# Kernel optimization log

Measured on AMD Instinct MI355X. Metric: run time of the kernel, lower is better.

The kernel has to match this reference:

```python
import jax, jax.numpy as jnp
import numpy as np

IMG, P, C = 512, 16, 1
D, DEPTH, H, DH, MLP = 768, 12, 8, 64, 2048
GRID = IMG // P          # 32
NP = GRID * GRID         # 1024 patches
N = NP + 1               # +cls token
EPS = 1e-5


def _ln(x, s, b):
    m = jnp.mean(x, -1, keepdims=True)
    v = jnp.mean((x - m) ** 2, -1, keepdims=True)
    return (x - m) * jax.lax.rsqrt(v + EPS) * s + b


def setup_inputs() -> dict:
    key = jax.random.key(0)
    ks = jax.random.split(key, 12)
    s = 0.02
    f32 = jnp.float32
    return {
        "x": jax.random.normal(ks[0], (4, C, IMG, IMG), f32),
        "conv_w": jax.random.normal(ks[1], (D, C, P, P), f32) * s,   # [out,in,kh,kw] like torch
        "conv_b": jnp.zeros((D,), f32),
        "cls_token": jax.random.normal(ks[2], (1, 1, D), f32),
        "pos_emb": jax.random.normal(ks[3], (1, N, D), f32),
        "qkv_w": jax.random.normal(ks[4], (DEPTH, D, 3 * H * DH), f32) * s,  # [in,out] layout
        "merge_w": jax.random.normal(ks[5], (DEPTH, H * DH, D), f32) * s,
        "merge_b": jnp.zeros((DEPTH, D), f32),
        "ln1_s": jnp.ones((DEPTH, D), f32),
        "ln1_b": jnp.zeros((DEPTH, D), f32),
        "ln2_s": jnp.ones((DEPTH, D), f32),
        "ln2_b": jnp.zeros((DEPTH, D), f32),
        "ffn_w1": jax.random.normal(ks[6], (DEPTH, D, MLP), f32) * s,
        "ffn_b1": jnp.zeros((DEPTH, MLP), f32),
        "ffn_w2": jax.random.normal(ks[7], (DEPTH, MLP, D), f32) * s,
        "ffn_b2": jnp.zeros((DEPTH, D), f32),
        "lnf_s": jnp.ones((D,), f32),
        "lnf_b": jnp.zeros((D,), f32),
    }


def reference(x, conv_w, conv_b, cls_token, pos_emb, qkv_w, merge_w, merge_b,
              ln1_s, ln1_b, ln2_s, ln2_b, ffn_w1, ffn_b1, ffn_w2, ffn_b2,
              lnf_s, lnf_b):
    B = x.shape[0]
    # Patch embed: stride-P conv == non-overlapping patch extraction + matmul
    xr = x.reshape(B, C, GRID, P, GRID, P)
    tok = jnp.einsum('bchpwq,dcpq->bhwd', xr, conv_w).reshape(B, NP, D) + conv_b
    t = jnp.concatenate([jnp.broadcast_to(cls_token, (B, 1, D)), tok], axis=1)
    t = t + pos_emb  # dropout is identity in eval
    scale = DH ** -0.5
    for i in range(DEPTH):
        # MSA with pre-LN
        h = _ln(t, ln1_s[i], ln1_b[i])
        qkv = (h @ qkv_w[i]).reshape(B, N, H, 3, DH)   # [B,N,H,3,DH]
        q = jnp.transpose(qkv[..., 0, :], (0, 2, 1, 3))  # [B,H,N,DH]
        k = jnp.transpose(qkv[..., 1, :], (0, 2, 1, 3))
        v = jnp.transpose(qkv[..., 2, :], (0, 2, 1, 3))
        att = jax.nn.softmax(jnp.einsum('bhnd,bhmd->bhnm', q, k) * scale, axis=-1)
        o = jnp.einsum('bhnm,bhmd->bhnd', att, v)
        o = jnp.transpose(o, (0, 2, 1, 3)).reshape(B, N, H * DH)
        t = t + (o @ merge_w[i] + merge_b[i])
        # FFN with pre-LN, exact (erf) GELU like torch nn.GELU
        h2 = _ln(t, ln2_s[i], ln2_b[i])
        f = jax.nn.gelu(h2 @ ffn_w1[i] + ffn_b1[i], approximate=False)
        t = t + (f @ ffn_w2[i] + ffn_b2[i])
    return _ln(t, lnf_s, lnf_b)
```

## Files before the change

### kernel.cpp

```cpp
#include <hip/hip_runtime.h>

#define DEV __device__ __forceinline__

typedef short s8v __attribute__((ext_vector_type(8)));
typedef float f4v __attribute__((ext_vector_type(4)));

DEV short f2bf(float f) {
  unsigned u = __float_as_uint(f);
  u += 0x7FFFu + ((u >> 16) & 1u);
  return (short)(u >> 16);
}
DEV short f2bf_fast(float f) {
  return (short)((__float_as_uint(f) + 0x8000u) >> 16);
}
DEV float bf2f(short s) { return __uint_as_float(((unsigned)(unsigned short)s) << 16); }

DEV void gld_lds16(const short* g, short* l) {
  __builtin_amdgcn_global_load_lds(
      (const __attribute__((address_space(1))) void*)g,
      (__attribute__((address_space(3))) void*)l, 16, 0, 0);
}

DEV int xcd_swz(int id, int nwg) {
  int q8 = nwg >> 3, r8 = nwg & 7, xcd = id & 7, off = id >> 3;
  return (xcd < r8) ? (xcd * (q8 + 1) + off) : (r8 * (q8 + 1) + (xcd - r8) * q8 + off);
}

template<int BN>
__global__ __launch_bounds__(256) void gemm_t(
    const short* __restrict__ A, const short* __restrict__ B, void* __restrict__ Cv,
    const float* __restrict__ bias,
    int M, int N, int K, int lda, int ldb, int ldc, int flags)
{
  constexpr int BPASS = BN / 32;
  constexpr int MI = (BN == 128) ? 4 : 2;
  __shared__ __align__(16) short As[2][64 * 64];
  __shared__ __align__(16) short Bs[2][BN * 64];
  int nwg = gridDim.x * gridDim.y;
  int idl = blockIdx.y * gridDim.x + blockIdx.x;
  int swz = xcd_swz(idl, nwg);
  int bx = swz % gridDim.x, by = swz / gridDim.x;
  int m0 = by * 64, n0 = bx * BN;
  int tid = threadIdx.x, lane = tid & 63, w = tid >> 6;
  int lr = lane & 15, kg = lane >> 4;
  int wrb = (BN == 128) ? 0 : (w >> 1) * 32;
  int wcb = (BN == 128) ? w * 32 : (w & 1) * 32;
  f4v acc[MI][2] = {};
  int NT = K >> 6;

#define STAGE(bufi, k0)                                                   \
  {                                                                       \
    _Pragma("unroll")                                                     \
    for (int p = 0; p < 2; ++p) {                                         \
      int ch = p * 256 + w * 64 + lane;                                   \
      int row = ch >> 3, c = (ch & 7) ^ (row & 7);                        \
      gld_lds16(A + (long)(m0 + row) * lda + (k0) + c * 8,                \
                &As[bufi][(p * 256 + w * 64) * 8]);                       \
    }                                                                     \
    _Pragma("unroll")                                                     \
    for (int p = 0; p < BPASS; ++p) {                                     \
      int ch = p * 256 + w * 64 + lane;                                   \
      int row = ch >> 3, c = (ch & 7) ^ (row & 7);                        \
      gld_lds16(B + (long)(n0 + row) * ldb + (k0) + c * 8,                \
                &Bs[bufi][(p * 256 + w * 64) * 8]);                       \
    }                                                                     \
  }

  STAGE(0, 0)
  for (int t = 0; t < NT; ++t) {
    int buf = t & 1;
    if (t + 1 < NT) {
      STAGE(buf ^ 1, (t + 1) * 64)
      if constexpr (BN == 128)
        asm volatile("s_waitcnt vmcnt(6)" ::: "memory");
      else
        asm volatile("s_waitcnt vmcnt(4)" ::: "memory");
    } else {
      asm volatile("s_waitcnt vmcnt(0)" ::: "memory");
    }
    __builtin_amdgcn_s_barrier();
    #pragma unroll
    for (int ks = 0; ks < 2; ++ks) {
      s8v av[MI], bv[2];
      #pragma unroll
      for (int mi = 0; mi < MI; ++mi) {
        int row = wrb + mi * 16 + lr;
        int sl = (ks * 4 + kg) ^ (row & 7);
        av[mi] = *(const s8v*)&As[buf][row * 64 + sl * 8];
      }
      #pragma unroll
      for (int ni = 0; ni < 2; ++ni) {
        int row = wcb + ni * 16 + lr;
        int sl = (ks * 4 + kg) ^ (row & 7);
        bv[ni] = *(const s8v*)&Bs[buf][row * 64 + sl * 8];
      }
      #pragma unroll
      for (int mi = 0; mi < MI; ++mi)
        #pragma unroll
        for (int ni = 0; ni < 2; ++ni)
          acc[mi][ni] = __builtin_amdgcn_mfma_f32_16x16x32_bf16(av[mi], bv[ni], acc[mi][ni], 0, 0, 0);
    }
    asm volatile("s_waitcnt lgkmcnt(0)" ::: "memory");
    __builtin_amdgcn_s_barrier();
  }
#undef STAGE

  float* Cf = (float*)Cv;
  short* Cb = (short*)Cv;
  #pragma unroll
  for (int mi = 0; mi < MI; ++mi)
    #pragma unroll
    for (int ni = 0; ni < 2; ++ni) {
      int col = n0 + wcb + ni * 16 + lr;
      float bvv = (flags & 1) ? bias[col] : 0.f;
      #pragma unroll
      for (int j = 0; j < 4; ++j) {
        int row = m0 + wrb + mi * 16 + kg * 4 + j;
        if (row >= M) continue;
        float v = acc[mi][ni][j] + bvv;
        if (flags & 2) v = 0.5f * v * (1.f + erff(v * 0.70710678118f));
        long ci = (long)row * ldc + col;
        if (flags & 8) Cb[ci] = f2bf(v);
        else { if (flags & 4) v += Cf[ci]; Cf[ci] = v; }
      }
    }
}

__global__ __launch_bounds__(256) void flash_k(
    const short* __restrict__ qkv, short* __restrict__ O)
{
  int swz = xcd_swz(blockIdx.x, 544);
  int z = swz / 17, qt = swz - z * 17;
  int zb = z >> 3, zh = z & 7;
  const short* base = qkv + (long)zb * 1025 * 1536 + zh * 192;
  const short* Qg = base;
  const short* Kg = base + 64;
  const short* Vg = base + 128;
  int q0 = qt * 64;
  int tid = threadIdx.x, lane = tid & 63, w = tid >> 6;
  int lr = lane & 15, kg = lane >> 4;

  __shared__ __align__(16) short QPs[64][72];
  __shared__ __align__(16) short Ks[2][64 * 64];
  __shared__ __align__(16) short Vt[2][64][72];

  for (int s = tid; s < 512; s += 256) {
    int row = s >> 3, ch = s & 7;
    s8v v = {};
    if (q0 + row < 1025) v = *(const s8v*)(Qg + (long)(q0 + row) * 1536 + ch * 8);
    *(s8v*)&QPs[row][ch * 8] = v;
  }
  __syncthreads();
  s8v aq[2];
  aq[0] = *(const s8v*)&QPs[w * 16 + lr][kg * 8];
  aq[1] = *(const s8v*)&QPs[w * 16 + lr][32 + kg * 8];

#define STAGE_K(bufi, kv0)                                                 \
  {                                                                        \
    int s0 = w * 128;                                                      \
    _Pragma("unroll")                                                      \
    for (int i = 0; i < 2; ++i) {                                          \
      int s = s0 + i * 64 + lane;                                          \
      int row = s >> 3, c = (s & 7) ^ (row & 7);                           \
      gld_lds16(Kg + (long)((kv0) + row) * 1536 + c * 8,                   \
                &Ks[bufi][(s0 + i * 64) * 8]);                             \
    }                                                                      \
  }

  f4v acc[4] = {};
  float m_run[4], l_run[4];
  #pragma unroll
  for (int j = 0; j < 4; ++j) { m_run[j] = -3.0e38f; l_run[j] = 0.f; }
  const float C2 = 0.18033688011112042f;

  STAGE_K(0, 0)
  #pragma unroll
  for (int p = 0; p < 2; ++p) {
    int s = p * 256 + tid;
    int key = s & 63, ch = s >> 6;
    s8v v = *(const s8v*)(Vg + (long)key * 1536 + ch * 8);
    #pragma unroll
    for (int j = 0; j < 8; ++j) Vt[0][ch * 8 + j][key] = v[j];
  }
  asm volatile("s_waitcnt vmcnt(0)" ::: "memory");
  asm volatile("s_waitcnt lgkmcnt(0)" ::: "memory");
  __builtin_amdgcn_s_barrier();

  for (int kt = 0; kt < 17; ++kt) {
    int cur = kt & 1;
    int kv0 = kt * 64;
    s8v vreg[2];
    int vok[2];
    if (kt < 16) {
      STAGE_K(cur ^ 1, kv0 + 64)
      #pragma unroll
      for (int p = 0; p < 2; ++p) {
        int s = p * 256 + tid;
        int key = (s & 63) + kv0 + 64, ch = s >> 6;
        vok[p] = key < 1025;
        vreg[p] = vok[p] ? *(const s8v*)(Vg + (long)key * 1536 + ch * 8) : s8v{};
      }
    }

    f4v sa[4] = {};
    __builtin_amdgcn_s_setprio(1);
    #pragma unroll
    for (int ni = 0; ni < 4; ++ni) {
      int row = ni * 16 + lr;
      #pragma unroll
      for (int ks = 0; ks < 2; ++ks) {
        int c = (ks * 4 + kg) ^ (row & 7);
        s8v bk = *(const s8v*)&Ks[cur][row * 64 + c * 8];
        sa[ni] = __builtin_amdgcn_mfma_f32_16x16x32_bf16(aq[ks], bk, sa[ni], 0, 0, 0);
      }
    }
    __builtin_amdgcn_s_setprio(0);
    float sv[4][4], pv[4][4], tm[4], ts[4];
    #pragma unroll
    for (int j = 0; j < 4; ++j) tm[j] = -3.0e38f;
    if (kt != 16) {
      #pragma unroll
      for (int ni = 0; ni < 4; ++ni)
        #pragma unroll
        for (int j = 0; j < 4; ++j) {
          float s = sa[ni][j] * C2;
          sv[ni][j] = s;
          tm[j] = fmaxf(tm[j], s);
        }
    } else {
      #pragma unroll
      for (int ni = 0; ni < 4; ++ni) {
        bool valid = (kv0 + ni * 16 + lr) < 1025;
        #pragma unroll
        for (int j = 0; j < 4; ++j) {
          float s = valid ? sa[ni][j] * C2 : -3.0e38f;
          sv[ni][j] = s;
          tm[j] = fmaxf(tm[j], s);
        }
      }
    }
    #pragma unroll
    for (int o = 1; o < 16; o <<= 1)
      #pragma unroll
      for (int j = 0; j < 4; ++j) tm[j] = fmaxf(tm[j], __shfl_xor(tm[j], o));
    float scale[4], m_new[4];
    #pragma unroll
    for (int j = 0; j < 4; ++j) {
      m_new[j] = fmaxf(m_run[j], tm[j]);
      scale[j] = exp2f(m_run[j] - m_new[j]);
      m_run[j] = m_new[j];
      ts[j] = 0.f;
    }
    #pragma unroll
    for (int ni = 0; ni < 4; ++ni)
      #pragma unroll
      for (int j = 0; j < 4; ++j) {
        float p = exp2f(sv[ni][j] - m_new[j]);
        pv[ni][j] = p;
        ts[j] += p;
      }
    #pragma unroll
    for (int o = 1; o < 16; o <<= 1)
      #pragma unroll
      for (int j = 0; j < 4; ++j) ts[j] += __shfl_xor(ts[j], o);
    #pragma unroll
    for (int j = 0; j < 4; ++j) l_run[j] = l_run[j] * scale[j] + ts[j];
    #pragma unroll
    for (int ni = 0; ni < 4; ++ni)
      #pragma unroll
      for (int j = 0; j < 4; ++j) acc[ni][j] *= scale[j];

    if (kt < 16) {
      #pragma unroll
      for (int p = 0; p < 2; ++p) {
        int s = p * 256 + tid;
        int key = s & 63, ch = s >> 6;
        s8v v = vok[p] ? vreg[p] : s8v{};
        #pragma unroll
        for (int j = 0; j < 8; ++j) Vt[cur ^ 1][ch * 8 + j][key] = v[j];
      }
    }

    #pragma unroll
    for (int ni = 0; ni < 4; ++ni)
      #pragma unroll
      for (int j = 0; j < 4; ++j)
        QPs[w * 16 + kg * 4 + j][ni * 16 + lr] = f2bf_fast(pv[ni][j]);
    asm volatile("s_waitcnt lgkmcnt(0)" ::: "memory");
    s8v ap[2];
    ap[0] = *(const s8v*)&QPs[w * 16 + lr][kg * 8];
    ap[1] = *(const s8v*)&QPs[w * 16 + lr][32 + kg * 8];
    __builtin_amdgcn_s_setprio(1);
    #pragma unroll
    for (int ni = 0; ni < 4; ++ni) {
      #pragma unroll
      for (int ks = 0; ks < 2; ++ks) {
        s8v bvv = *(const s8v*)&Vt[cur][ni * 16 + lr][ks * 32 + kg * 8];
        acc[ni] = __builtin_amdgcn_mfma_f32_16x16x32_bf16(ap[ks], bvv, acc[ni], 0, 0, 0);
      }
    }
    __builtin_amdgcn_s_setprio(0);
    asm volatile("s_waitcnt lgkmcnt(0)" ::: "memory");
    asm volatile("s_waitcnt vmcnt(0)" ::: "memory");
    __builtin_amdgcn_s_barrier();
  }
#undef STAGE_K

  float inv[4];
  #pragma unroll
  for (int j = 0; j < 4; ++j) inv[j] = 1.f / l_run[j];
  #pragma unroll
  for (int ni = 0; ni < 4; ++ni)
    #pragma unroll
    for (int j = 0; j < 4; ++j) {
      int row = q0 + w * 16 + kg * 4 + j;
      if (row < 1025)
        O[((long)(zb * 1025 + row)) * 512 + zh * 64 + ni * 16 + lr] = f2bf(acc[ni][j] * inv[j]);
    }
}

DEV void tconv_body(const float* w, short* wt, int K, int N, int bx, int by, int tid)
{
  __shared__ float tile[32][33];
  int n0 = bx * 32, k0 = by * 32;
  int tx = tid & 31, ty = tid >> 5;
  #pragma unroll
  for (int j = 0; j < 4; ++j)
    tile[ty + j * 8][tx] = w[(long)(k0 + ty + j * 8) * N + n0 + tx];
  __syncthreads();
  #pragma unroll
  for (int j = 0; j < 4; ++j)
    wt[(long)(n0 + ty + j * 8) * K + k0 + tx] = f2bf(tile[tx][ty + j * 8]);
}

__global__ __launch_bounds__(256) void tconv4_k(
    const float* __restrict__ sq, const float* __restrict__ sm,
    const float* __restrict__ sf1, const float* __restrict__ sf2,
    short* __restrict__ dq, short* __restrict__ dm,
    short* __restrict__ df1, short* __restrict__ df2)
{
  int id = blockIdx.x, tid = threadIdx.x;
  if (id < 1152)       tconv_body(sq,  dq,  768, 1536, id % 48,          id / 48,          tid);
  else if (id < 1536)  tconv_body(sm,  dm,  512, 768,  (id - 1152) % 24, (id - 1152) / 24, tid);
  else if (id < 3072)  tconv_body(sf1, df1, 768, 2048, (id - 1536) % 64, (id - 1536) / 64, tid);
  else                 tconv_body(sf2, df2, 2048, 768, (id - 3072) % 24, (id - 3072) / 24, tid);
}

__global__ __launch_bounds__(256) void cvt_k(const float* __restrict__ in,
    short* __restrict__ out, int n)
{
  int i = blockIdx.x * 256 + threadIdx.x;
  if (i < n) out[i] = f2bf(in[i]);
}

DEV void st_ln(float* p, float v) { *p = v; }
DEV void st_ln(short* p, float v) { *p = f2bf(v); }

template<typename OT>
__global__ __launch_bounds__(256) void ln_k(const float* __restrict__ x,
    const float* __restrict__ g, const float* __restrict__ b,
    OT* __restrict__ y, int rows)
{
  int row = blockIdx.x;
  if (row >= rows) return;
  const float* xr = x + (long)row * 768;
  OT* yr = y + (long)row * 768;
  int t = threadIdx.x;
  float v0 = xr[t], v1 = xr[t + 256], v2 = xr[t + 512];
  float s = v0 + v1 + v2, s2 = v0 * v0 + v1 * v1 + v2 * v2;
  #pragma unroll
  for (int o = 32; o > 0; o >>= 1) { s += __shfl_down(s, o); s2 += __shfl_down(s2, o); }
  __shared__ float as_[4], as2_[4];
  if ((t & 63) == 0) { as_[t >> 6] = s; as2_[t >> 6] = s2; }
  __syncthreads();
  s = as_[0] + as_[1] + as_[2] + as_[3];
  s2 = as2_[0] + as2_[1] + as2_[2] + as2_[3];
  float mean = s * (1.f / 768.f);
  float var = s2 * (1.f / 768.f) - mean * mean;
  float r = rsqrtf(var + 1e-5f);
  st_ln(&yr[t],       (v0 - mean) * r * g[t]       + b[t]);
  st_ln(&yr[t + 256], (v1 - mean) * r * g[t + 256] + b[t + 256]);
  st_ln(&yr[t + 512], (v2 - mean) * r * g[t + 512] + b[t + 512]);
}

__global__ __launch_bounds__(256) void im2col_k(const float* __restrict__ x,
    short* __restrict__ A)
{
  int i = blockIdx.x * 256 + threadIdx.x;
  int k = i & 255, row = i >> 8;
  int px = k & 15, py = k >> 4;
  int gx = row & 31, gy = (row >> 5) & 31, b = row >> 10;
  A[i] = f2bf(x[((long)(b * 512) + gy * 16 + py) * 512 + gx * 16 + px]);
}

__global__ __launch_bounds__(256) void assemble_k(const short* __restrict__ tok,
    const float* __restrict__ cls, const float* __restrict__ pos, float* __restrict__ t)
{
  int i = blockIdx.x * 256 + threadIdx.x;
  int d = i % 768; int rn = i / 768; int n = rn % 1025; int b = rn / 1025;
  float v = (n == 0) ? cls[d] : bf2f(tok[((long)(b * 1024 + n - 1)) * 768 + d]);
  t[i] = v + pos[n * 768 + d];
}

extern "C" void kernel_launch(void* const* d_in, const int* in_sizes, int n_in,
                              void* d_out, int out_size, void* d_ws, size_t ws_size,
                              hipStream_t stream)
{
  const float* x       = (const float*)d_in[0];
  const float* conv_w  = (const float*)d_in[1];
  const float* conv_b  = (const float*)d_in[2];
  const float* cls     = (const float*)d_in[3];
  const float* pos     = (const float*)d_in[4];
  const float* qkv_w   = (const float*)d_in[5];
  const float* merge_w = (const float*)d_in[6];
  const float* merge_b = (const float*)d_in[7];
  const float* ln1_s   = (const float*)d_in[8];
  const float* ln1_b   = (const float*)d_in[9];
  const float* ln2_s   = (const float*)d_in[10];
  const float* ln2_b   = (const float*)d_in[11];
  const float* ffn_w1  = (const float*)d_in[12];
  const float* ffn_b1  = (const float*)d_in[13];
  const float* ffn_w2  = (const float*)d_in[14];
  const float* ffn_b2  = (const float*)d_in[15];
  const float* lnf_s   = (const float*)d_in[16];
  const float* lnf_b   = (const float*)d_in[17];

  char* wsp = (char*)d_ws;
  size_t o = 0;
  auto take = [&](size_t bytes) { char* r = wsp + o; o = (o + bytes + 255) & ~(size_t)255; return r; };
  short* wq   = (short*)take(1536ul * 768 * 2);
  short* wm   = (short*)take(768ul * 512 * 2);
  short* wf1  = (short*)take(2048ul * 768 * 2);
  short* wf2  = (short*)take(768ul * 2048 * 2);
  short* wcv  = (short*)take(768ul * 256 * 2);
  float* t    = (float*)take(4100ul * 768 * 4);
  char*  hO   = take(4352ul * 768 * 2);
  short* qkv  = (short*)take(4ul * 1025 * 1536 * 2);
  char*  fV   = take(4352ul * 2048 * 2);
  take(2ul << 20);

  short* h   = (short*)hO;
  short* O   = (short*)hO;
  short* f   = (short*)fV;
  short* imc = (short*)fV;
  short* tok = (short*)(fV + 4096ul * 256 * 2);

  dim3 blk(256);

  cvt_k<<<768, blk, 0, stream>>>(conv_w, wcv, 768 * 256);
  im2col_k<<<4096, blk, 0, stream>>>(x, imc);
  gemm_t<64><<<dim3(12, 64), blk, 0, stream>>>(imc, wcv, tok, conv_b,
      4096, 768, 256, 256, 256, 768, 1 | 8);
  assemble_k<<<12300, blk, 0, stream>>>(tok, cls, pos, t);

  for (int i = 0; i < 12; ++i) {
    tconv4_k<<<4608, blk, 0, stream>>>(
        qkv_w + (long)i * 768 * 1536, merge_w + (long)i * 512 * 768,
        ffn_w1 + (long)i * 768 * 2048, ffn_w2 + (long)i * 2048 * 768,
        wq, wm, wf1, wf2);

    ln_k<short><<<4100, blk, 0, stream>>>(t, ln1_s + i * 768, ln1_b + i * 768, h, 4100);
    gemm_t<128><<<dim3(12, 65), blk, 0, stream>>>(h, wq, qkv, nullptr,
        4100, 1536, 768, 768, 768, 1536, 8);
    flash_k<<<544, blk, 0, stream>>>(qkv, O);
    gemm_t<64><<<dim3(12, 65), blk, 0, stream>>>(O, wm, t, merge_b + i * 768,
        4100, 768, 512, 512, 512, 768, 1 | 4);
    ln_k<short><<<4100, blk, 0, stream>>>(t, ln2_s + i * 768, ln2_b + i * 768, h, 4100);
    gemm_t<128><<<dim3(16, 65), blk, 0, stream>>>(h, wf1, f, ffn_b1 + i * 2048,
        4100, 2048, 768, 768, 768, 2048, 1 | 2 | 8);
    gemm_t<64><<<dim3(12, 65), blk, 0, stream>>>(f, wf2, t, ffn_b2 + i * 768,
        4100, 768, 2048, 2048, 2048, 768, 1 | 4);
  }
  ln_k<float><<<4100, blk, 0, stream>>>(t, lnf_s, lnf_b, (float*)d_out, 4100);
}
```

Baseline: 2.297 ms.

## Compute transposed attention scores and pass probabilities through lane shuffles

Flash attention now computes S^T by swapping the MFMA operands, so each lane owns one query's scores. Row max and row sum then need only two cross-lane shuffles instead of four rounds over four rows. The P matrix is packed to bf16 and redistributed into the A-operand layout with __shfl, removing the LDS write, wait and read round trip. Q fragments are loaded straight from global memory, dropping the QPs staging buffer and a barrier. In exchange, the last query tile now reads past row 1025 without a bounds check, and extra shuffles are added for the rescale and normalisation factors.

Result: faster. 2.134 ms (-7.1%).

```diff
diff --git a/kernel.cpp b/kernel.cpp
--- a/kernel.cpp
+++ b/kernel.cpp
@@ -140,20 +140,15 @@
   int tid = threadIdx.x, lane = tid & 63, w = tid >> 6;
   int lr = lane & 15, kg = lane >> 4;
 
-  __shared__ __align__(16) short QPs[64][72];
   __shared__ __align__(16) short Ks[2][64 * 64];
   __shared__ __align__(16) short Vt[2][64][72];
 
-  for (int s = tid; s < 512; s += 256) {
-    int row = s >> 3, ch = s & 7;
-    s8v v = {};
-    if (q0 + row < 1025) v = *(const s8v*)(Qg + (long)(q0 + row) * 1536 + ch * 8);
-    *(s8v*)&QPs[row][ch * 8] = v;
-  }
-  __syncthreads();
   s8v aq[2];
-  aq[0] = *(const s8v*)&QPs[w * 16 + lr][kg * 8];
-  aq[1] = *(const s8v*)&QPs[w * 16 + lr][32 + kg * 8];
+  {
+    long qrow = q0 + w * 16 + lr;
+    aq[0] = *(const s8v*)(Qg + qrow * 1536 + kg * 8);
+    aq[1] = *(const s8v*)(Qg + qrow * 1536 + 32 + kg * 8);
+  }
 
 #define STAGE_K(bufi, kv0)                                                 \
   {                                                                        \
@@ -168,9 +163,7 @@
   }
 
   f4v acc[4] = {};
-  float m_run[4], l_run[4];
-  #pragma unroll
-  for (int j = 0; j < 4; ++j) { m_run[j] = -3.0e38f; l_run[j] = 0.f; }
+  float m_run = -3.0e38f, l_run = 0.f;
   const float C2 = 0.18033688011112042f;
 
   STAGE_K(0, 0)
@@ -210,65 +203,57 @@
       #pragma unroll
       for (int ks = 0; ks < 2; ++ks) {
         int c = (ks * 4 + kg) ^ (row & 7);
-        s8v bk = *(const s8v*)&Ks[cur][row * 64 + c * 8];
-        sa[ni] = __builtin_amdgcn_mfma_f32_16x16x32_bf16(aq[ks], bk, sa[ni], 0, 0, 0);
+        s8v kf = *(const s8v*)&Ks[cur][row * 64 + c * 8];
+        sa[ni] = __builtin_amdgcn_mfma_f32_16x16x32_bf16(kf, aq[ks], sa[ni], 0, 0, 0);
       }
     }
     __builtin_amdgcn_s_setprio(0);
-    float sv[4][4], pv[4][4], tm[4], ts[4];
-    #pragma unroll
-    for (int j = 0; j < 4; ++j) tm[j] = -3.0e38f;
+
+    float sv[4][4], pv[4][4];
+    float tm = -3.0e38f;
     if (kt != 16) {
       #pragma unroll
       for (int ni = 0; ni < 4; ++ni)
         #pragma unroll
-        for (int j = 0; j < 4; ++j) {
-          float s = sa[ni][j] * C2;
-          sv[ni][j] = s;
-          tm[j] = fmaxf(tm[j], s);
+        for (int jj = 0; jj < 4; ++jj) {
+          float s = sa[ni][jj] * C2;
+          sv[ni][jj] = s;
+          tm = fmaxf(tm, s);
         }
     } else {
       #pragma unroll
-      for (int ni = 0; ni < 4; ++ni) {
-        bool valid = (kv0 + ni * 16 + lr) < 1025;
+      for (int ni = 0; ni < 4; ++ni)
         #pragma unroll
-        for (int j = 0; j < 4; ++j) {
-          float s = valid ? sa[ni][j] * C2 : -3.0e38f;
-          sv[ni][j] = s;
-          tm[j] = fmaxf(tm[j], s);
-        }
-      }
-    }
-    #pragma unroll
-    for (int o = 1; o < 16; o <<= 1)
-      #pragma unroll
-      for (int j = 0; j < 4; ++j) tm[j] = fmaxf(tm[j], __shfl_xor(tm[j], o));
-    float scale[4], m_new[4];
-    #pragma unroll
-    for (int j = 0; j < 4; ++j) {
-      m_new[j] = fmaxf(m_run[j], tm[j]);
-      scale[j] = exp2f(m_run[j] - m_new[j]);
-      m_run[j] = m_new[j];
-      ts[j] = 0.f;
-    }
+        for (int jj = 0; jj < 4; ++jj) sv[ni][jj] = -3.0e38f;
+      if (kg == 0) sv[0][0] = sa[0][0] * C2;
+      tm = sv[0][0];
+    }
+    tm = fmaxf(tm, __shfl_xor(tm, 16));
+    tm = fmaxf(tm, __shfl_xor(tm, 32));
+    float m_new = fmaxf(m_run, tm);
+    float scale = exp2f(m_run - m_new);
+    m_run = m_new;
+    float ts = 0.f;
     #pragma unroll
     for (int ni = 0; ni < 4; ++ni)
       #pragma unroll
-      for (int j = 0; j < 4; ++j) {
-        float p = exp2f(sv[ni][j] - m_new[j]);
-        pv[ni][j] = p;
-        ts[j] += p;
-      }
-    #pragma unroll
-    for (int o = 1; o < 16; o <<= 1)
-      #pragma unroll
-      for (int j = 0; j < 4; ++j) ts[j] += __shfl_xor(ts[j], o);
-    #pragma unroll
-    for (int j = 0; j < 4; ++j) l_run[j] = l_run[j] * scale[j] + ts[j];
+      for (int jj = 0; jj < 4; ++jj) {
+        float p = exp2f(sv[ni][jj] - m_new);
+        pv[ni][jj] = p;
+        ts += p;
+      }
+    ts += __shfl_xor(ts, 16);
+    ts += __shfl_xor(ts, 32);
+    l_run = l_run * scale + ts;
+
+    float scq[4];
+    #pragma unroll
+    for (int jj = 0; jj < 4; ++jj)
+      scq[jj] = __shfl(scale, kg * 4 + jj + 16 * kg);
     #pragma unroll
     for (int ni = 0; ni < 4; ++ni)
       #pragma unroll
-      for (int j = 0; j < 4; ++j) acc[ni][j] *= scale[j];
+      for (int jj = 0; jj < 4; ++jj) acc[ni][jj] *= scq[jj];
 
     if (kt < 16) {
       #pragma unroll
@@ -281,22 +266,32 @@
       }
     }
 
+    unsigned pr[4][2];
     #pragma unroll
     for (int ni = 0; ni < 4; ++ni)
       #pragma unroll
-      for (int j = 0; j < 4; ++j)
-        QPs[w * 16 + kg * 4 + j][ni * 16 + lr] = f2bf_fast(pv[ni][j]);
-    asm volatile("s_waitcnt lgkmcnt(0)" ::: "memory");
-    s8v ap[2];
-    ap[0] = *(const s8v*)&QPs[w * 16 + lr][kg * 8];
-    ap[1] = *(const s8v*)&QPs[w * 16 + lr][32 + kg * 8];
+      for (int h = 0; h < 2; ++h) {
+        unsigned lo = (unsigned)(unsigned short)f2bf_fast(pv[ni][2 * h]);
+        unsigned hi = (unsigned)(unsigned short)f2bf_fast(pv[ni][2 * h + 1]);
+        pr[ni][h] = lo | (hi << 16);
+      }
+    union PU { s8v v; unsigned u[4]; };
+    PU apu[2];
+    #pragma unroll
+    for (int ks = 0; ks < 2; ++ks)
+      #pragma unroll
+      for (int t = 0; t < 4; ++t) {
+        unsigned src = (kg & 2) ? pr[2 * ks + 1][t & 1] : pr[2 * ks][t & 1];
+        apu[ks].u[t] = __shfl(src, lr + 16 * (2 * (kg & 1) + (t >> 1)));
+      }
+
     __builtin_amdgcn_s_setprio(1);
     #pragma unroll
     for (int ni = 0; ni < 4; ++ni) {
       #pragma unroll
       for (int ks = 0; ks < 2; ++ks) {
         s8v bvv = *(const s8v*)&Vt[cur][ni * 16 + lr][ks * 32 + kg * 8];
-        acc[ni] = __builtin_amdgcn_mfma_f32_16x16x32_bf16(ap[ks], bvv, acc[ni], 0, 0, 0);
+        acc[ni] = __builtin_amdgcn_mfma_f32_16x16x32_bf16(apu[ks].v, bvv, acc[ni], 0, 0, 0);
       }
     }
     __builtin_amdgcn_s_setprio(0);
@@ -306,16 +301,18 @@
   }
 #undef STAGE_K
 
-  float inv[4];
-  #pragma unroll
-  for (int j = 0; j < 4; ++j) inv[j] = 1.f / l_run[j];
+  float linv = 1.f / l_run;
+  float invq[4];
+  #pragma unroll
+  for (int jj = 0; jj < 4; ++jj)
+    invq[jj] = __shfl(linv, kg * 4 + jj + 16 * kg);
   #pragma unroll
   for (int ni = 0; ni < 4; ++ni)
     #pragma unroll
-    for (int j = 0; j < 4; ++j) {
-      int row = q0 + w * 16 + kg * 4 + j;
+    for (int jj = 0; jj < 4; ++jj) {
+      int row = q0 + w * 16 + kg * 4 + jj;
       if (row < 1025)
-        O[((long)(zb * 1025 + row)) * 512 + zh * 64 + ni * 16 + lr] = f2bf(acc[ni][j] * inv[j]);
+        O[((long)(zb * 1025 + row)) * 512 + zh * 64 + ni * 16 + lr] = f2bf(acc[ni][jj] * invq[jj]);
     }
 }
 
```
